# Kernel optimization log

Hardware: AMD Instinct MI355X
Metric: run time of the kernel (lower is better)

Reference implementation:

```python
import jax, jax.numpy as jnp
import numpy as np

DIM = 64
M_DIM = 16
EDGE_DIM = 0
IN_DIM = 2 * DIM + EDGE_DIM + 1  # 129


def _mlp(x, W1, b1, W2, b2):
    return jax.nn.relu(x @ W1 + b1) @ W2 + b2


def setup_inputs() -> dict:
    key = jax.random.key(0)
    ks = jax.random.split(key, 10)
    s = 0.02
    inp = {
        "feats": jax.random.normal(ks[0], (1, 1024, DIM), dtype=jnp.float32),
        "coors": jax.random.normal(ks[1], (1, 1024, 3), dtype=jnp.float32),
        # edge_mlp: Linear(129,258) -> ReLU -> Linear(258,16)
        "eW1": jax.random.normal(ks[2], (IN_DIM, IN_DIM * 2), dtype=jnp.float32) * s,
        "eb1": jnp.zeros((IN_DIM * 2,), jnp.float32),
        "eW2": jax.random.normal(ks[3], (IN_DIM * 2, M_DIM), dtype=jnp.float32) * s,
        "eb2": jnp.zeros((M_DIM,), jnp.float32),
        # coors_mlp: Linear(16,64) -> ReLU -> Linear(64,1)
        "cW1": jax.random.normal(ks[4], (M_DIM, M_DIM * 4), dtype=jnp.float32) * s,
        "cb1": jnp.zeros((M_DIM * 4,), jnp.float32),
        "cW2": jax.random.normal(ks[5], (M_DIM * 4, 1), dtype=jnp.float32) * s,
        "cb2": jnp.zeros((1,), jnp.float32),
        # hidden_mlp: Linear(80,128) -> ReLU -> Linear(128,64)
        "hW1": jax.random.normal(ks[6], (DIM + M_DIM, DIM * 2), dtype=jnp.float32) * s,
        "hb1": jnp.zeros((DIM * 2,), jnp.float32),
        "hW2": jax.random.normal(ks[7], (DIM * 2, DIM), dtype=jnp.float32) * s,
        "hb2": jnp.zeros((DIM,), jnp.float32),
    }
    return inp


def reference(feats, coors, eW1, eb1, eW2, eb2, cW1, cb1, cW2, cb2, hW1, hb1, hW2, hb2):
    b, n, d = feats.shape
    # all-pairs relative coordinates and distances: (b, n, n, 3), (b, n, n, 1)
    rel_coors = coors[:, :, None, :] - coors[:, None, :, :]
    rel_dist = jnp.linalg.norm(rel_coors, axis=-1, keepdims=True)
    feats_i = jnp.broadcast_to(feats[:, :, None, :], (b, n, n, d))
    feats_j = jnp.broadcast_to(feats[:, None, :, :], (b, n, n, d))
    edge_input = jnp.concatenate([feats_i, feats_j, rel_dist], axis=-1)  # (b,n,n,2d+1)
    m_ij = _mlp(edge_input, eW1, eb1, eW2, eb2)                          # (b,n,n,m_dim)
    coor_weights = _mlp(m_ij, cW1, cb1, cW2, cb2)[..., 0]                # (b,n,n)
    coors_out = jnp.einsum('bij,bijc->bic', coor_weights, rel_coors)     # (b,n,3)
    m_i = m_ij.sum(axis=-2)                                              # (b,n,m_dim)
    hidden_out = _mlp(jnp.concatenate([feats, m_i], axis=-1), hW1, hb1, hW2, hb2)
    return (hidden_out, coors_out)
```

## Files before the change

kernel.cpp:

```cpp
#include <hip/hip_runtime.h>
#include <hip/hip_bf16.h>
#include <stdint.h>

#define N 1024
#define DIM 64
#define MDIM 16
#define EH 258
#define EHP 264
#define CH 64
#define HH 128
#define PRE_ROWS 8

typedef __bf16 bf16x8 __attribute__((ext_vector_type(8)));
typedef float f32x4 __attribute__((ext_vector_type(4)));
typedef uint32_t u32x4 __attribute__((ext_vector_type(4)));
union B8 { uint32_t u[4]; bf16x8 v; };

__device__ __forceinline__ uint32_t cvtpk(float lo, float hi) {
  uint32_t r;
  asm("v_cvt_pk_bf16_f32 %0, %1, %2" : "=v"(r) : "v"(lo), "v"(hi));
  return r;
}
__device__ __forceinline__ float bflo(uint32_t u) { return __uint_as_float(u << 16); }
__device__ __forceinline__ float bfhi(uint32_t u) { return __uint_as_float(u & 0xffff0000u); }

__global__ __launch_bounds__(256) void eg_pre(
    const float* __restrict__ feats, const float* __restrict__ eW1,
    const float* __restrict__ eb1,
    float* __restrict__ A, __hip_bfloat16* __restrict__ Bb)
{
  __shared__ float sf[PRE_ROWS][DIM];
  int ib = blockIdx.x, t = threadIdx.x;
  for (int q = t; q < PRE_ROWS * DIM; q += 256)
    sf[q >> 6][q & 63] = feats[ib * PRE_ROWS * DIM + q];
  __syncthreads();
  for (int k = t; k < EH; k += 256) {
    float bias = eb1[k];
    float a[PRE_ROWS], bv[PRE_ROWS];
#pragma unroll
    for (int ii = 0; ii < PRE_ROWS; ++ii) { a[ii] = bias; bv[ii] = 0.f; }
#pragma unroll 4
    for (int d = 0; d < DIM; ++d) {
      float wt = eW1[d * EH + k];
      float wb = eW1[(DIM + d) * EH + k];
#pragma unroll
      for (int ii = 0; ii < PRE_ROWS; ++ii) {
        a[ii]  = fmaf(sf[ii][d], wt, a[ii]);
        bv[ii] = fmaf(sf[ii][d], wb, bv[ii]);
      }
    }
#pragma unroll
    for (int ii = 0; ii < PRE_ROWS; ++ii) {
      A[(ib * PRE_ROWS + ii) * EH + k] = a[ii];
      Bb[(ib * PRE_ROWS + ii) * EHP + k] = __float2bfloat16(bv[ii]);
    }
  }
}

__global__ __launch_bounds__(256, 2) void eg_main(
    const float* __restrict__ feats, const float* __restrict__ coors,
    const float* __restrict__ eW1, const float* __restrict__ eW2,
    const float* __restrict__ eb2, const float* __restrict__ cW1,
    const float* __restrict__ cb1, const float* __restrict__ cW2,
    const float* __restrict__ cb2, const float* __restrict__ hW1,
    const float* __restrict__ hb1, const float* __restrict__ hW2,
    const float* __restrict__ hb2,
    const float* __restrict__ A, const __hip_bfloat16* __restrict__ Bb,
    float* __restrict__ out)
{
  __shared__ float sEW2f[EH * MDIM];
  __shared__ __align__(16) float sA[EHP];
  __shared__ __align__(16) float sW3[EHP];
  __shared__ float sCB1[CH], sCW2[CH], sEB2[MDIM], sFeat[DIM];
  __shared__ float4 sRel4[N];
  __shared__ union {
    float cw1[MDIM * CH];
    struct { float redm[4][16]; float redc[4][3]; float mi[MDIM]; float hid[HH]; } e;
  } sU;

  const int i = blockIdx.x, t = threadIdx.x;
  const int lane = t & 63, wv = t >> 6;
  const int r16 = lane & 15, g = lane >> 4;

  for (int q = t; q < EH * MDIM; q += 256) sEW2f[q] = eW2[q];
  for (int q = t; q < EH; q += 256) { sA[q] = A[i * EH + q]; sW3[q] = eW1[128 * EH + q]; }
  for (int q = t; q < MDIM * CH; q += 256) sU.cw1[q] = cW1[q];
  if (t < CH)   { sCB1[t] = cb1[t]; sCW2[t] = cW2[t]; }
  if (t < MDIM) sEB2[t] = eb2[t];
  if (t < DIM)  sFeat[t] = feats[i * DIM + t];
  {
    float cx = coors[i * 3], cy = coors[i * 3 + 1], cz = coors[i * 3 + 2];
    const float4* c4 = (const float4*)coors;
    float4 ca = c4[t * 3 + 0], cb = c4[t * 3 + 1], cc = c4[t * 3 + 2];
    float jx[4] = {ca.x, ca.w, cb.z, cc.y};
    float jy[4] = {ca.y, cb.x, cb.w, cc.z};
    float jz[4] = {ca.z, cb.y, cc.x, cc.w};
#pragma unroll
    for (int q = 0; q < 4; ++q) {
      float rx = cx - jx[q], ry = cy - jy[q], rz = cz - jz[q];
      float d = sqrtf(fmaf(rx, rx, fmaf(ry, ry, rz * rz)));
      sRel4[t * 4 + q] = make_float4(rx, ry, rz, d);
    }
  }
  __syncthreads();

  f32x4 eb2r;
#pragma unroll
  for (int r = 0; r < 4; ++r) eb2r[r] = sEB2[4 * g + r];
  float tw0[4], tw1[4];
#pragma unroll
  for (int r = 0; r < 4; ++r) {
    tw0[r] = sEW2f[256 * MDIM + 4 * g + r];
    tw1[r] = sEW2f[257 * MDIM + 4 * g + r];
  }
  float a256 = sA[256], a257 = sA[257], w356 = sW3[256], w357 = sW3[257];
  float cb2v = cb2[0];
  B8 fcw1[4];
#pragma unroll
  for (int T = 0; T < 4; ++T) {
    float cv[8];
#pragma unroll
    for (int e = 0; e < 8; ++e)
      cv[e] = (g < 2) ? sU.cw1[(8 * g + e) * CH + 16 * T + r16] : 0.f;
    fcw1[T].u[0] = cvtpk(cv[0], cv[1]); fcw1[T].u[1] = cvtpk(cv[2], cv[3]);
    fcw1[T].u[2] = cvtpk(cv[4], cv[5]); fcw1[T].u[3] = cvtpk(cv[6], cv[7]);
  }
  __syncthreads();

  const f32x4* sA4 = (const f32x4*)sA;
  const f32x4* sW34 = (const f32x4*)sW3;
  const char* Bbyte = (const char*)Bb;

  float macc[4] = {0.f, 0.f, 0.f, 0.f};
  float cax = 0.f, cay = 0.f, caz = 0.f;

  for (int p = 0; p < 2; ++p) {
    const int jb = wv * 16 + p * 512;
    float djp[8];
    f32x4 D[8];
#pragma unroll
    for (int tt = 0; tt < 8; ++tt) {
      djp[tt] = sRel4[jb + tt * 64 + r16].w;
      D[tt] = eb2r;
    }

    for (int s = 0; s < 8; ++s) {
      const int kb = s * 32 + g * 8;
      u32x4 bq[8];
#pragma unroll
      for (int tt = 0; tt < 8; ++tt)
        bq[tt] = *(const u32x4*)(Bbyte + (size_t)((jb + tt * 64 + r16) * (EHP * 2) + kb * 2));
      f32x4 af0 = sA4[(kb >> 2)], af1 = sA4[(kb >> 2) + 1];
      f32x4 wf0 = sW34[(kb >> 2)], wf1 = sW34[(kb >> 2) + 1];
      float fe[8];
#pragma unroll
      for (int e = 0; e < 8; ++e) fe[e] = sEW2f[(kb + e) * MDIM + r16];
      B8 few;
      few.u[0] = cvtpk(fe[0], fe[1]); few.u[1] = cvtpk(fe[2], fe[3]);
      few.u[2] = cvtpk(fe[4], fe[5]); few.u[3] = cvtpk(fe[6], fe[7]);

#pragma unroll
      for (int tt = 0; tt < 8; ++tt) {
        float hh[8];
#pragma unroll
        for (int e = 0; e < 8; ++e) {
          uint32_t u = bq[tt][e >> 1];
          float b = (e & 1) ? bfhi(u) : bflo(u);
          float av = (e < 4) ? af0[e & 3] : af1[e & 3];
          float wv3 = (e < 4) ? wf0[e & 3] : wf1[e & 3];
          hh[e] = fmaxf(fmaf(djp[tt], wv3, av + b), 0.f);
        }
        B8 hb;
        hb.u[0] = cvtpk(hh[0], hh[1]); hb.u[1] = cvtpk(hh[2], hh[3]);
        hb.u[2] = cvtpk(hh[4], hh[5]); hb.u[3] = cvtpk(hh[6], hh[7]);
        D[tt] = __builtin_amdgcn_mfma_f32_16x16x32_bf16(few.v, hb.v, D[tt], 0, 0, 0);
      }
    }

#pragma unroll
    for (int tt = 0; tt < 8; ++tt) {
      const int j = jb + tt * 64 + r16;
      float4 rl = sRel4[j];
      uint32_t bt = *(const uint32_t*)(Bbyte + (size_t)(j * (EHP * 2) + 512));
      float h6 = fmaxf(fmaf(rl.w, w356, a256 + bflo(bt)), 0.f);
      float h7 = fmaxf(fmaf(rl.w, w357, a257 + bfhi(bt)), 0.f);
#pragma unroll
      for (int r = 0; r < 4; ++r) {
        D[tt][r] = fmaf(h6, tw0[r], D[tt][r]);
        D[tt][r] = fmaf(h7, tw1[r], D[tt][r]);
        macc[r] += D[tt][r];
      }
      uint32_t p0 = cvtpk(D[tt][0], D[tt][1]);
      uint32_t p1 = cvtpk(D[tt][2], D[tt][3]);
      int s0 = r16 + (((2 * g) & 3) << 4);
      int s1 = r16 + (((2 * g + 1) & 3) << 4);
      uint32_t b0 = (uint32_t)__shfl((int)p0, s0, 64);
      uint32_t b1 = (uint32_t)__shfl((int)p1, s0, 64);
      uint32_t b2 = (uint32_t)__shfl((int)p0, s1, 64);
      uint32_t b3 = (uint32_t)__shfl((int)p1, s1, 64);
      B8 mf;
      mf.u[0] = (g < 2) ? b0 : 0u; mf.u[1] = (g < 2) ? b1 : 0u;
      mf.u[2] = (g < 2) ? b2 : 0u; mf.u[3] = (g < 2) ? b3 : 0u;
      float wacc = 0.f;
#pragma unroll
      for (int T = 0; T < 4; ++T) {
        f32x4 cbv;
#pragma unroll
        for (int r = 0; r < 4; ++r) cbv[r] = sCB1[16 * T + 4 * g + r];
        f32x4 hd = __builtin_amdgcn_mfma_f32_16x16x32_bf16(fcw1[T].v, mf.v, cbv, 0, 0, 0);
#pragma unroll
        for (int r = 0; r < 4; ++r)
          wacc = fmaf(fmaxf(hd[r], 0.f), sCW2[16 * T + 4 * g + r], wacc);
      }
      wacc += __shfl_xor(wacc, 16, 64);
      wacc += __shfl_xor(wacc, 32, 64);
      float w = cb2v + wacc;
      cax = fmaf(w, rl.x, cax); cay = fmaf(w, rl.y, cay); caz = fmaf(w, rl.z, caz);
    }
  }

#pragma unroll
  for (int off = 1; off < 16; off <<= 1) {
#pragma unroll
    for (int r = 0; r < 4; ++r) macc[r] += __shfl_xor(macc[r], off, 64);
    cax += __shfl_xor(cax, off, 64);
    cay += __shfl_xor(cay, off, 64);
    caz += __shfl_xor(caz, off, 64);
  }
  if (r16 == 0) {
#pragma unroll
    for (int r = 0; r < 4; ++r) sU.e.redm[wv][4 * g + r] = macc[r];
    if (g == 0) { sU.e.redc[wv][0] = cax; sU.e.redc[wv][1] = cay; sU.e.redc[wv][2] = caz; }
  }
  __syncthreads();
  if (t < MDIM)
    sU.e.mi[t] = sU.e.redm[0][t] + sU.e.redm[1][t] + sU.e.redm[2][t] + sU.e.redm[3][t];
  if (t >= 16 && t < 19) {
    int c = t - 16;
    out[N * DIM + i * 3 + c] =
        sU.e.redc[0][c] + sU.e.redc[1][c] + sU.e.redc[2][c] + sU.e.redc[3][c];
  }
  __syncthreads();

  if (t < HH) {
    float acc = hb1[t];
#pragma unroll 8
    for (int d = 0; d < DIM; ++d) acc = fmaf(sFeat[d], hW1[d * HH + t], acc);
#pragma unroll
    for (int d = 0; d < MDIM; ++d) acc = fmaf(sU.e.mi[d], hW1[(DIM + d) * HH + t], acc);
    sU.e.hid[t] = fmaxf(acc, 0.f);
  }
  __syncthreads();
  if (t < DIM) {
    float acc = hb2[t];
#pragma unroll 8
    for (int c = 0; c < HH; ++c) acc = fmaf(sU.e.hid[c], hW2[c * DIM + t], acc);
    out[i * DIM + t] = acc;
  }
}

extern "C" void kernel_launch(void* const* d_in, const int* in_sizes, int n_in,
                              void* d_out, int out_size, void* d_ws, size_t ws_size,
                              hipStream_t stream) {
  const float* feats = (const float*)d_in[0];
  const float* coors = (const float*)d_in[1];
  const float* eW1   = (const float*)d_in[2];
  const float* eb1   = (const float*)d_in[3];
  const float* eW2   = (const float*)d_in[4];
  const float* eb2   = (const float*)d_in[5];
  const float* cW1   = (const float*)d_in[6];
  const float* cb1   = (const float*)d_in[7];
  const float* cW2   = (const float*)d_in[8];
  const float* cb2   = (const float*)d_in[9];
  const float* hW1   = (const float*)d_in[10];
  const float* hb1   = (const float*)d_in[11];
  const float* hW2   = (const float*)d_in[12];
  const float* hb2   = (const float*)d_in[13];

  float* A = (float*)d_ws;
  __hip_bfloat16* Bb = (__hip_bfloat16*)((char*)d_ws + (size_t)N * EH * 4);
  float* out = (float*)d_out;

  eg_pre<<<N / PRE_ROWS, 256, 0, stream>>>(feats, eW1, eb1, A, Bb);
  eg_main<<<N, 256, 0, stream>>>(feats, coors, eW1, eW2, eb2, cW1, cb1, cW2, cb2,
                                 hW1, hb1, hW2, hb2, A, Bb, out);
}
```

Baseline: 160.6 us.

## Raise eg_main occupancy, pad eW2 smem, use packed f32 math in hidden layer

```diff
diff --git a/kernel.cpp b/kernel.cpp
--- a/kernel.cpp
+++ b/kernel.cpp
@@ -13,12 +13,23 @@
 
 typedef __bf16 bf16x8 __attribute__((ext_vector_type(8)));
 typedef float f32x4 __attribute__((ext_vector_type(4)));
+typedef float f32x2 __attribute__((ext_vector_type(2)));
 typedef uint32_t u32x4 __attribute__((ext_vector_type(4)));
 union B8 { uint32_t u[4]; bf16x8 v; };
 
 __device__ __forceinline__ uint32_t cvtpk(float lo, float hi) {
   uint32_t r;
   asm("v_cvt_pk_bf16_f32 %0, %1, %2" : "=v"(r) : "v"(lo), "v"(hi));
+  return r;
+}
+__device__ __forceinline__ f32x2 pk_add(f32x2 a, f32x2 b) {
+  f32x2 r;
+  asm("v_pk_add_f32 %0, %1, %2" : "=v"(r) : "v"(a), "v"(b));
+  return r;
+}
+__device__ __forceinline__ f32x2 pk_fma(f32x2 a, f32x2 b, f32x2 c) {
+  f32x2 r;
+  asm("v_pk_fma_f32 %0, %1, %2, %3" : "=v"(r) : "v"(a), "v"(b), "v"(c));
   return r;
 }
 __device__ __forceinline__ float bflo(uint32_t u) { return __uint_as_float(u << 16); }
@@ -57,7 +68,7 @@
   }
 }
 
-__global__ __launch_bounds__(256, 2) void eg_main(
+__global__ __launch_bounds__(256, 4) void eg_main(
     const float* __restrict__ feats, const float* __restrict__ coors,
     const float* __restrict__ eW1, const float* __restrict__ eW2,
     const float* __restrict__ eb2, const float* __restrict__ cW1,
@@ -68,23 +79,21 @@
     const float* __restrict__ A, const __hip_bfloat16* __restrict__ Bb,
     float* __restrict__ out)
 {
-  __shared__ float sEW2f[EH * MDIM];
   __shared__ __align__(16) float sA[EHP];
   __shared__ __align__(16) float sW3[EHP];
-  __shared__ float sCB1[CH], sCW2[CH], sEB2[MDIM], sFeat[DIM];
-  __shared__ float4 sRel4[N];
-  __shared__ union {
-    float cw1[MDIM * CH];
-    struct { float redm[4][16]; float redc[4][3]; float mi[MDIM]; float hid[HH]; } e;
-  } sU;
+  __shared__ float sEW2p[EH * 17];
+  __shared__ __align__(16) float4 sRel4[N];
+  __shared__ __align__(16) float sCB1[CH];
+  __shared__ __align__(16) float sCW2[CH];
+  __shared__ float sEB2[MDIM], sFeat[DIM];
+  __shared__ struct { float redm[4][16]; float redc[4][3]; float mi[MDIM]; float hid[HH]; } sE;
 
   const int i = blockIdx.x, t = threadIdx.x;
   const int lane = t & 63, wv = t >> 6;
   const int r16 = lane & 15, g = lane >> 4;
 
-  for (int q = t; q < EH * MDIM; q += 256) sEW2f[q] = eW2[q];
+  for (int q = t; q < EH * MDIM; q += 256) sEW2p[(q >> 4) * 17 + (q & 15)] = eW2[q];
   for (int q = t; q < EH; q += 256) { sA[q] = A[i * EH + q]; sW3[q] = eW1[128 * EH + q]; }
-  for (int q = t; q < MDIM * CH; q += 256) sU.cw1[q] = cW1[q];
   if (t < CH)   { sCB1[t] = cb1[t]; sCW2[t] = cW2[t]; }
   if (t < MDIM) sEB2[t] = eb2[t];
   if (t < DIM)  sFeat[t] = feats[i * DIM + t];
@@ -102,6 +111,17 @@
       sRel4[t * 4 + q] = make_float4(rx, ry, rz, d);
     }
   }
+  B8 fcw1[4];
+#pragma unroll
+  for (int T = 0; T < 4; ++T) {
+    float cv[8];
+#pragma unroll
+    for (int e = 0; e < 8; ++e)
+      cv[e] = (g < 2) ? cW1[(8 * g + e) * CH + 16 * T + r16] : 0.f;
+    fcw1[T].u[0] = cvtpk(cv[0], cv[1]); fcw1[T].u[1] = cvtpk(cv[2], cv[3]);
+    fcw1[T].u[2] = cvtpk(cv[4], cv[5]); fcw1[T].u[3] = cvtpk(cv[6], cv[7]);
+  }
+  float cb2v = cb2[0];
   __syncthreads();
 
   f32x4 eb2r;
@@ -110,73 +130,63 @@
   float tw0[4], tw1[4];
 #pragma unroll
   for (int r = 0; r < 4; ++r) {
-    tw0[r] = sEW2f[256 * MDIM + 4 * g + r];
-    tw1[r] = sEW2f[257 * MDIM + 4 * g + r];
+    tw0[r] = sEW2p[256 * 17 + 4 * g + r];
+    tw1[r] = sEW2p[257 * 17 + 4 * g + r];
   }
   float a256 = sA[256], a257 = sA[257], w356 = sW3[256], w357 = sW3[257];
-  float cb2v = cb2[0];
-  B8 fcw1[4];
-#pragma unroll
-  for (int T = 0; T < 4; ++T) {
-    float cv[8];
-#pragma unroll
-    for (int e = 0; e < 8; ++e)
-      cv[e] = (g < 2) ? sU.cw1[(8 * g + e) * CH + 16 * T + r16] : 0.f;
-    fcw1[T].u[0] = cvtpk(cv[0], cv[1]); fcw1[T].u[1] = cvtpk(cv[2], cv[3]);
-    fcw1[T].u[2] = cvtpk(cv[4], cv[5]); fcw1[T].u[3] = cvtpk(cv[6], cv[7]);
-  }
-  __syncthreads();
-
-  const f32x4* sA4 = (const f32x4*)sA;
-  const f32x4* sW34 = (const f32x4*)sW3;
+
+  const f32x2* sA2 = (const f32x2*)sA;
+  const f32x2* sW32 = (const f32x2*)sW3;
   const char* Bbyte = (const char*)Bb;
+  const int ewb = g * 136 + r16;
 
   float macc[4] = {0.f, 0.f, 0.f, 0.f};
   float cax = 0.f, cay = 0.f, caz = 0.f;
 
+#pragma unroll 1
   for (int p = 0; p < 2; ++p) {
     const int jb = wv * 16 + p * 512;
     float djp[8];
     f32x4 D[8];
+    const char* brow[8];
 #pragma unroll
     for (int tt = 0; tt < 8; ++tt) {
       djp[tt] = sRel4[jb + tt * 64 + r16].w;
       D[tt] = eb2r;
-    }
-
+      brow[tt] = Bbyte + (size_t)((jb + tt * 64 + r16) * (EHP * 2) + g * 16);
+    }
+
+#pragma unroll
     for (int s = 0; s < 8; ++s) {
-      const int kb = s * 32 + g * 8;
-      u32x4 bq[8];
-#pragma unroll
-      for (int tt = 0; tt < 8; ++tt)
-        bq[tt] = *(const u32x4*)(Bbyte + (size_t)((jb + tt * 64 + r16) * (EHP * 2) + kb * 2));
-      f32x4 af0 = sA4[(kb >> 2)], af1 = sA4[(kb >> 2) + 1];
-      f32x4 wf0 = sW34[(kb >> 2)], wf1 = sW34[(kb >> 2) + 1];
-      float fe[8];
-#pragma unroll
-      for (int e = 0; e < 8; ++e) fe[e] = sEW2f[(kb + e) * MDIM + r16];
+      f32x2 a2[4], w2[4];
+#pragma unroll
+      for (int q = 0; q < 4; ++q) {
+        a2[q] = sA2[16 * s + 4 * g + q];
+        w2[q] = sW32[16 * s + 4 * g + q];
+      }
       B8 few;
-      few.u[0] = cvtpk(fe[0], fe[1]); few.u[1] = cvtpk(fe[2], fe[3]);
-      few.u[2] = cvtpk(fe[4], fe[5]); few.u[3] = cvtpk(fe[6], fe[7]);
-
+#pragma unroll
+      for (int h = 0; h < 4; ++h)
+        few.u[h] = cvtpk(sEW2p[ewb + s * 544 + (2 * h) * 17],
+                         sEW2p[ewb + s * 544 + (2 * h + 1) * 17]);
 #pragma unroll
       for (int tt = 0; tt < 8; ++tt) {
-        float hh[8];
-#pragma unroll
-        for (int e = 0; e < 8; ++e) {
-          uint32_t u = bq[tt][e >> 1];
-          float b = (e & 1) ? bfhi(u) : bflo(u);
-          float av = (e < 4) ? af0[e & 3] : af1[e & 3];
-          float wv3 = (e < 4) ? wf0[e & 3] : wf1[e & 3];
-          hh[e] = fmaxf(fmaf(djp[tt], wv3, av + b), 0.f);
+        u32x4 bq = *(const u32x4*)(brow[tt] + s * 64);
+        f32x2 dd; dd[0] = djp[tt]; dd[1] = djp[tt];
+        B8 hb;
+#pragma unroll
+        for (int q = 0; q < 4; ++q) {
+          f32x2 bp; bp[0] = bflo(bq[q]); bp[1] = bfhi(bq[q]);
+          f32x2 hv = pk_add(bp, a2[q]);
+          hv = pk_fma(dd, w2[q], hv);
+          hb.u[q] = cvtpk(fmaxf(hv[0], 0.f), fmaxf(hv[1], 0.f));
         }
-        B8 hb;
-        hb.u[0] = cvtpk(hh[0], hh[1]); hb.u[1] = cvtpk(hh[2], hh[3]);
-        hb.u[2] = cvtpk(hh[4], hh[5]); hb.u[3] = cvtpk(hh[6], hh[7]);
         D[tt] = __builtin_amdgcn_mfma_f32_16x16x32_bf16(few.v, hb.v, D[tt], 0, 0, 0);
       }
     }
 
+    const f32x4* cb14 = (const f32x4*)sCB1;
+    const f32x4* cw24 = (const f32x4*)sCW2;
 #pragma unroll
     for (int tt = 0; tt < 8; ++tt) {
       const int j = jb + tt * 64 + r16;
@@ -204,13 +214,12 @@
       float wacc = 0.f;
 #pragma unroll
       for (int T = 0; T < 4; ++T) {
-        f32x4 cbv;
-#pragma unroll
-        for (int r = 0; r < 4; ++r) cbv[r] = sCB1[16 * T + 4 * g + r];
+        f32x4 cbv = cb14[4 * T + g];
         f32x4 hd = __builtin_amdgcn_mfma_f32_16x16x32_bf16(fcw1[T].v, mf.v, cbv, 0, 0, 0);
+        f32x4 cwv = cw24[4 * T + g];
 #pragma unroll
         for (int r = 0; r < 4; ++r)
-          wacc = fmaf(fmaxf(hd[r], 0.f), sCW2[16 * T + 4 * g + r], wacc);
+          wacc = fmaf(fmaxf(hd[r], 0.f), cwv[r], wacc);
       }
       wacc += __shfl_xor(wacc, 16, 64);
       wacc += __shfl_xor(wacc, 32, 64);
@@ -229,16 +238,15 @@
   }
   if (r16 == 0) {
 #pragma unroll
-    for (int r = 0; r < 4; ++r) sU.e.redm[wv][4 * g + r] = macc[r];
-    if (g == 0) { sU.e.redc[wv][0] = cax; sU.e.redc[wv][1] = cay; sU.e.redc[wv][2] = caz; }
+    for (int r = 0; r < 4; ++r) sE.redm[wv][4 * g + r] = macc[r];
+    if (g == 0) { sE.redc[wv][0] = cax; sE.redc[wv][1] = cay; sE.redc[wv][2] = caz; }
   }
   __syncthreads();
   if (t < MDIM)
-    sU.e.mi[t] = sU.e.redm[0][t] + sU.e.redm[1][t] + sU.e.redm[2][t] + sU.e.redm[3][t];
+    sE.mi[t] = sE.redm[0][t] + sE.redm[1][t] + sE.redm[2][t] + sE.redm[3][t];
   if (t >= 16 && t < 19) {
     int c = t - 16;
-    out[N * DIM + i * 3 + c] =
-        sU.e.redc[0][c] + sU.e.redc[1][c] + sU.e.redc[2][c] + sU.e.redc[3][c];
+    out[N * DIM + i * 3 + c] = sE.redc[0][c] + sE.redc[1][c] + sE.redc[2][c] + sE.redc[3][c];
   }
   __syncthreads();
 
@@ -247,14 +255,14 @@
 #pragma unroll 8
     for (int d = 0; d < DIM; ++d) acc = fmaf(sFeat[d], hW1[d * HH + t], acc);
 #pragma unroll
-    for (int d = 0; d < MDIM; ++d) acc = fmaf(sU.e.mi[d], hW1[(DIM + d) * HH + t], acc);
-    sU.e.hid[t] = fmaxf(acc, 0.f);
+    for (int d = 0; d < MDIM; ++d) acc = fmaf(sE.mi[d], hW1[(DIM + d) * HH + t], acc);
+    sE.hid[t] = fmaxf(acc, 0.f);
   }
   __syncthreads();
   if (t < DIM) {
     float acc = hb2[t];
 #pragma unroll 8
-    for (int c = 0; c < HH; ++c) acc = fmaf(sU.e.hid[c], hW2[c * DIM + t], acc);
+    for (int c = 0; c < HH; ++c) acc = fmaf(sE.hid[c], hW2[c * DIM + t], acc);
     out[i * DIM + t] = acc;
   }
 }
```

Result: slower. 207.4 us (+29.2%).
